# Kernel optimization log

Hardware: AMD Instinct MI355X
Metric: run time of the kernel (lower is better)

## Reference

```python
import jax, jax.numpy as jnp
import numpy as np

PART = 6
FEAT = 1024
DIM_CUT = 8
DC = FEAT // DIM_CUT  # 128
BATCH = 8192
NEG = -1000000.0
LRELU_SLOPE = 0.25
BN_EPS = 1e-5
L2_EPS = 1e-8


def lrelu(x):
    return jnp.where(x >= 0, x, LRELU_SLOPE * x)


def l2norm(x, axis=1):
    n = jnp.sqrt(jnp.sum(x * x, axis=axis, keepdims=True))
    return x / (n + L2_EPS)


def setup_inputs() -> dict:
    key = jax.random.key(0)
    ks = jax.random.split(key, 5)
    x = jax.random.normal(ks[0], (BATCH, FEAT, PART), dtype=jnp.float32)
    w_ps = jax.random.normal(ks[1], (PART, DC, FEAT), dtype=jnp.float32) * 0.02
    w_cs = jax.random.normal(ks[2], (PART, DC, FEAT), dtype=jnp.float32) * 0.02
    w_up = jax.random.normal(ks[3], (PART, FEAT, DC), dtype=jnp.float32) * 0.02
    w_la = jax.random.normal(ks[4], (PART, 512, FEAT), dtype=jnp.float32) * 0.02
    bn_gamma = jnp.ones((PART, FEAT), dtype=jnp.float32)
    bn_beta = jnp.zeros((PART, FEAT), dtype=jnp.float32)
    bn_mean = jnp.zeros((PART, FEAT), dtype=jnp.float32)
    bn_var = jnp.ones((PART, FEAT), dtype=jnp.float32)
    return {"x": x, "w_ps": w_ps, "w_cs": w_cs, "w_up": w_up,
            "bn_gamma": bn_gamma, "bn_beta": bn_beta,
            "bn_mean": bn_mean, "bn_var": bn_var, "w_la": w_la}


def reference(x, w_ps, w_cs, w_up, bn_gamma, bn_beta, bn_mean, bn_var, w_la):
    # x: [B, C=1024, P]. Per-part 1x1 convs == per-part matmuls, batched via einsum.
    ps = lrelu(jnp.einsum('bcp,pkc->bkp', x, w_ps))   # [B, 128, P]
    cs = lrelu(jnp.einsum('bcp,pkc->bkp', x, w_cs))   # [B, 128, P]
    ps_n = l2norm(ps, axis=1)
    cs_n = l2norm(cs, axis=1)
    # masked self-attention over parts
    att = jnp.einsum('bkp,bkq->bpq', ps_n, cs_n)       # [B, P, P]
    att = att + (jnp.eye(PART, dtype=att.dtype) * NEG)[None]
    att = jax.nn.softmax(att, axis=1)                  # torch F.softmax(dim=1)
    emb_att = jnp.einsum('bkp,bpq->bkq', ps_n, att)    # [B, 128, P]
    # per-part up-dim conv + BN(eval) + LReLU
    h = jnp.einsum('bkp,pok->bop', emb_att, w_up)      # [B, 1024, P]
    inv = 1.0 / jnp.sqrt(bn_var + BN_EPS)              # [P, 1024]
    h = (h - bn_mean.T[None]) * (bn_gamma * inv).T[None] + bn_beta.T[None]
    h = lrelu(h)
    emb2 = x + h                                       # residual, [B, 1024, P]
    # per-part local-attention conv (no BN / relu)
    out = jnp.einsum('bcp,poc->bop', emb2, w_la)       # [B, 512, P]
    return out
```

## Files before the change

kernel.cpp:

```cpp
#include <hip/hip_runtime.h>
#include <cstdint>
#include <cstddef>

#define B_N  8192
#define FEAT 1024
#define PART 6
#define DC   128
#define OUTC 512

typedef __bf16 bf16;
typedef bf16 bf16x8 __attribute__((ext_vector_type(8)));
typedef bf16 bf16x2 __attribute__((ext_vector_type(2)));
typedef float f32x4 __attribute__((ext_vector_type(4)));

__device__ __forceinline__ void gload16(const bf16* g, bf16* l) {
  __builtin_amdgcn_global_load_lds(
      (const __attribute__((address_space(1))) void*)g,
      (__attribute__((address_space(3))) void*)l, 16, 0, 0);
}

__global__ void k_prep(const float* __restrict__ w_ps, const float* __restrict__ w_cs,
                       const float* __restrict__ w_up, const float* __restrict__ w_la,
                       const float* __restrict__ g, const float* __restrict__ be,
                       const float* __restrict__ m, const float* __restrict__ v,
                       bf16* __restrict__ wpsb, bf16* __restrict__ wupb,
                       bf16* __restrict__ wlab, float* __restrict__ bnsc,
                       float* __restrict__ bnsh) {
  int i = blockIdx.x * 256 + threadIdx.x;
  const int NW = PART * DC * FEAT;
  const int NL = PART * OUTC * FEAT;
  if (i < NW) {
    int z = i / (DC * FEAT), r = i % (DC * FEAT);
    wpsb[(size_t)(2 * z) * DC * FEAT + r] = (bf16)w_ps[i];
    wpsb[(size_t)(2 * z + 1) * DC * FEAT + r] = (bf16)w_cs[i];
    wupb[i] = (bf16)w_up[i];
  }
  if (i < NL) wlab[i] = (bf16)w_la[i];
  if (i < PART * FEAT) {
    float inv = 1.0f / sqrtf(v[i] + 1e-5f);
    float s = g[i] * inv;
    bnsc[i] = s;
    bnsh[i] = be[i] - m[i] * s;
  }
}

__global__ void k_transpose_x(const float* __restrict__ x, bf16* __restrict__ xT) {
  int t = blockIdx.x * 256 + threadIdx.x;
  int b = t >> 9;
  int c0 = (t & 511) << 1;
  const float4* src = (const float4*)(x + ((size_t)b * FEAT + c0) * PART);
  float4 v0 = src[0], v1 = src[1], v2 = src[2];
  float e[12] = {v0.x, v0.y, v0.z, v0.w, v1.x, v1.y, v1.z, v1.w, v2.x, v2.y, v2.z, v2.w};
#pragma unroll
  for (int p = 0; p < PART; ++p) {
    bf16x2 w; w.x = (bf16)e[p]; w.y = (bf16)e[6 + p];
    *(bf16x2*)(xT + ((size_t)p * B_N + b) * FEAT + c0) = w;
  }
}

template <int EPI, int K, int N, int TM, int TN, int NZ>
__global__ __launch_bounds__(256) void k_gemm(
    const bf16* __restrict__ Abase, const bf16* __restrict__ Wbase,
    bf16* __restrict__ Out,
    const float* __restrict__ bnsc, const float* __restrict__ bnsh,
    const bf16* __restrict__ resid) {
  __shared__ bf16 As[128 * 64];
  __shared__ bf16 Ws[128 * 64];
  const int tid = threadIdx.x;
  const int wv = tid >> 6, lane = tid & 63;
  const int wr = wv >> 1, wc = wv & 1;
  const int l = lane & 15, hh = lane >> 4;

  constexpr int NWG = TM * TN * NZ;
  constexpr int QC = NWG / 8;
  int bid = blockIdx.x;
  int lid = (bid & 7) * QC + (bid >> 3);
  int tn = lid % TN;
  int tm = (lid / TN) % TM;
  int z = lid / (TN * TM);

  const bf16* A = Abase + (size_t)z * B_N * K + (size_t)tm * 128 * K;
  const bf16* W = Wbase + (size_t)z * N * K + (size_t)tn * 128 * K;

  f32x4 acc[4][4] = {};

  for (int kt = 0; kt < K / 64; ++kt) {
    __syncthreads();
#pragma unroll
    for (int it = 0; it < 4; ++it) {
      int s = it * 256 + wv * 64 + lane;
      int r = s >> 3;
      int c = (s & 7) ^ (r & 7);
      gload16(A + (size_t)r * K + kt * 64 + c * 8, &As[(it * 256 + wv * 64) * 8]);
      gload16(W + (size_t)r * K + kt * 64 + c * 8, &Ws[(it * 256 + wv * 64) * 8]);
    }
    asm volatile("s_waitcnt vmcnt(0)" ::: "memory");
    __syncthreads();
#pragma unroll
    for (int kk = 0; kk < 2; ++kk) {
      bf16x8 af[4], wf[4];
#pragma unroll
      for (int mi = 0; mi < 4; ++mi) {
        int row = wr * 64 + mi * 16 + l;
        int c = (kk * 4 + hh) ^ (row & 7);
        af[mi] = *(const bf16x8*)&As[row * 64 + c * 8];
      }
#pragma unroll
      for (int ni = 0; ni < 4; ++ni) {
        int row = wc * 64 + ni * 16 + l;
        int c = (kk * 4 + hh) ^ (row & 7);
        wf[ni] = *(const bf16x8*)&Ws[row * 64 + c * 8];
      }
#pragma unroll
      for (int mi = 0; mi < 4; ++mi)
#pragma unroll
        for (int ni = 0; ni < 4; ++ni)
          acc[mi][ni] = __builtin_amdgcn_mfma_f32_16x16x32_bf16(af[mi], wf[ni], acc[mi][ni], 0, 0, 0);
    }
  }

#pragma unroll
  for (int mi = 0; mi < 4; ++mi)
#pragma unroll
    for (int ni = 0; ni < 4; ++ni)
#pragma unroll
      for (int r = 0; r < 4; ++r) {
        int row = tm * 128 + wr * 64 + mi * 16 + hh * 4 + r;
        int col = tn * 128 + wc * 64 + ni * 16 + l;
        float v = acc[mi][ni][r];
        if constexpr (EPI == 0) {
          v = v >= 0.f ? v : 0.25f * v;
        } else if constexpr (EPI == 1) {
          v = v * bnsc[z * N + col] + bnsh[z * N + col];
          v = v >= 0.f ? v : 0.25f * v;
          v += (float)resid[((size_t)z * B_N + row) * N + col];
        }
        Out[((size_t)z * B_N + row) * N + col] = (bf16)v;
      }
}

__global__ __launch_bounds__(256) void k_att(const bf16* __restrict__ psb,
                                             bf16* __restrict__ embT) {
  int wv = threadIdx.x >> 6, lane = threadIdx.x & 63;
  int b = blockIdx.x * 4 + wv;
  float p0[6], p1[6], c0[6], c1[6];
#pragma unroll
  for (int p = 0; p < 6; ++p) {
    const bf16* base = psb + ((size_t)p * B_N + b) * 256;
    bf16x2 v = *(const bf16x2*)(base + 2 * lane);
    p0[p] = (float)v.x; p1[p] = (float)v.y;
    bf16x2 u = *(const bf16x2*)(base + 128 + 2 * lane);
    c0[p] = (float)u.x; c1[p] = (float)u.y;
  }
  float red[48];
#pragma unroll
  for (int p = 0; p < 6; ++p) {
    red[p] = p0[p] * p0[p] + p1[p] * p1[p];
    red[6 + p] = c0[p] * c0[p] + c1[p] * c1[p];
  }
#pragma unroll
  for (int p = 0; p < 6; ++p)
#pragma unroll
    for (int q = 0; q < 6; ++q)
      red[12 + p * 6 + q] = p0[p] * c0[q] + p1[p] * c1[q];
#pragma unroll
  for (int m = 1; m < 64; m <<= 1)
#pragma unroll
    for (int i = 0; i < 48; ++i)
      red[i] += __shfl_xor(red[i], m, 64);

  float inp[6], inc[6];
#pragma unroll
  for (int p = 0; p < 6; ++p) {
    inp[p] = 1.f / (sqrtf(red[p]) + 1e-8f);
    inc[p] = 1.f / (sqrtf(red[6 + p]) + 1e-8f);
  }
  float att[6][6];
#pragma unroll
  for (int p = 0; p < 6; ++p)
#pragma unroll
    for (int q = 0; q < 6; ++q)
      att[p][q] = red[12 + p * 6 + q] * inp[p] * inc[q] + (p == q ? -1000000.f : 0.f);
#pragma unroll
  for (int q = 0; q < 6; ++q) {
    float mx = att[0][q];
#pragma unroll
    for (int p = 1; p < 6; ++p) mx = fmaxf(mx, att[p][q]);
    float e[6], s = 0.f;
#pragma unroll
    for (int p = 0; p < 6; ++p) { e[p] = expf(att[p][q] - mx); s += e[p]; }
    float is = 1.f / s;
#pragma unroll
    for (int p = 0; p < 6; ++p) att[p][q] = e[p] * is;
  }
#pragma unroll
  for (int q = 0; q < 6; ++q) {
    float e0 = 0.f, e1 = 0.f;
#pragma unroll
    for (int p = 0; p < 6; ++p) {
      float a = att[p][q] * inp[p];
      e0 += p0[p] * a; e1 += p1[p] * a;
    }
    bf16x2 w; w.x = (bf16)e0; w.y = (bf16)e1;
    *(bf16x2*)(embT + ((size_t)q * B_N + b) * DC + 2 * lane) = w;
  }
}

__global__ void k_transpose_out(const bf16* __restrict__ oT, float* __restrict__ out) {
  int t = blockIdx.x * 256 + threadIdx.x;
  int b = t >> 8;
  int o0 = (t & 255) << 1;
  float a[6], c[6];
#pragma unroll
  for (int p = 0; p < 6; ++p) {
    bf16x2 v = *(const bf16x2*)(oT + ((size_t)p * B_N + b) * OUTC + o0);
    a[p] = (float)v.x; c[p] = (float)v.y;
  }
  float* dst = out + ((size_t)b * OUTC + o0) * PART;
  float4 w0 = {a[0], a[1], a[2], a[3]};
  float4 w1 = {a[4], a[5], c[0], c[1]};
  float4 w2 = {c[2], c[3], c[4], c[5]};
  ((float4*)dst)[0] = w0; ((float4*)dst)[1] = w1; ((float4*)dst)[2] = w2;
}

extern "C" void kernel_launch(void* const* d_in, const int* in_sizes, int n_in,
                              void* d_out, int out_size, void* d_ws, size_t ws_size,
                              hipStream_t stream) {
  const float* x    = (const float*)d_in[0];
  const float* w_ps = (const float*)d_in[1];
  const float* w_cs = (const float*)d_in[2];
  const float* w_up = (const float*)d_in[3];
  const float* gam  = (const float*)d_in[4];
  const float* bet  = (const float*)d_in[5];
  const float* mea  = (const float*)d_in[6];
  const float* var  = (const float*)d_in[7];
  const float* w_la = (const float*)d_in[8];

  char* ws = (char*)d_ws;
  size_t off = 0;
  auto alloc = [&](size_t bytes) { void* p = ws + off; off += (bytes + 255) & ~(size_t)255; return p; };

  bf16* xT    = (bf16*)alloc((size_t)PART * B_N * FEAT * 2);
  bf16* wpsb  = (bf16*)alloc((size_t)PART * 256 * FEAT * 2);
  bf16* wupb  = (bf16*)alloc((size_t)PART * FEAT * DC * 2);
  bf16* wlab  = (bf16*)alloc((size_t)PART * OUTC * FEAT * 2);
  float* bnsc = (float*)alloc((size_t)PART * FEAT * 4);
  float* bnsh = (float*)alloc((size_t)PART * FEAT * 4);
  bf16* psb   = (bf16*)alloc((size_t)PART * B_N * 256 * 2);
  bf16* embT  = (bf16*)alloc((size_t)PART * B_N * DC * 2);
  bf16* emb2T = (bf16*)alloc((size_t)PART * B_N * FEAT * 2);
  bf16* outT  = xT;

  k_prep<<<(PART * OUTC * FEAT + 255) / 256, 256, 0, stream>>>(
      w_ps, w_cs, w_up, w_la, gam, bet, mea, var, wpsb, wupb, wlab, bnsc, bnsh);
  k_transpose_x<<<B_N * 512 / 256, 256, 0, stream>>>(x, xT);

  k_gemm<0, FEAT, 256, 64, 2, 6><<<768, 256, 0, stream>>>(
      xT, wpsb, psb, nullptr, nullptr, nullptr);
  k_att<<<B_N / 4, 256, 0, stream>>>(psb, embT);
  k_gemm<1, DC, FEAT, 64, 8, 6><<<3072, 256, 0, stream>>>(
      embT, wupb, emb2T, bnsc, bnsh, xT);
  k_gemm<2, FEAT, OUTC, 64, 4, 6><<<1536, 256, 0, stream>>>(
      emb2T, wlab, outT, nullptr, nullptr, nullptr);
  k_transpose_out<<<B_N * 256 / 256, 256, 0, stream>>>(outT, (float*)d_out);
}
```

Before: 615.9 us.

## Double-buffer GEMM K-loop, fuse prep kernels, pack two batches per wave in attention

The GEMM main loop now uses two 32-wide K buffers in LDS. It prefetches the next tile with partial vmcnt waits and raw s_barrier, and drops the XOR swizzle for a layout split by half-wave. It also sets launch_bounds occupancy to 3. The weight-prep and x-transpose kernels are merged into one launch. The attention kernel packs two batch rows per wave with 4-element vector loads, halving the shuffle reduction depth, and uses fast __expf. The risks are LDS bank conflicts from the unswizzled layout and more barriers per K step.

Result: no change. 624.8 us (+1.5%).

```diff
diff --git a/kernel.cpp b/kernel.cpp
--- a/kernel.cpp
+++ b/kernel.cpp
@@ -10,6 +10,7 @@
 
 typedef __bf16 bf16;
 typedef bf16 bf16x8 __attribute__((ext_vector_type(8)));
+typedef bf16 bf16x4 __attribute__((ext_vector_type(4)));
 typedef bf16 bf16x2 __attribute__((ext_vector_type(2)));
 typedef float f32x4 __attribute__((ext_vector_type(4)));
 
@@ -19,53 +20,53 @@
       (__attribute__((address_space(3))) void*)l, 16, 0, 0);
 }
 
-__global__ void k_prep(const float* __restrict__ w_ps, const float* __restrict__ w_cs,
-                       const float* __restrict__ w_up, const float* __restrict__ w_la,
-                       const float* __restrict__ g, const float* __restrict__ be,
-                       const float* __restrict__ m, const float* __restrict__ v,
-                       bf16* __restrict__ wpsb, bf16* __restrict__ wupb,
-                       bf16* __restrict__ wlab, float* __restrict__ bnsc,
-                       float* __restrict__ bnsh) {
-  int i = blockIdx.x * 256 + threadIdx.x;
+__global__ void k_preptx(const float* __restrict__ x, bf16* __restrict__ xT,
+                         const float* __restrict__ w_ps, const float* __restrict__ w_cs,
+                         const float* __restrict__ w_up, const float* __restrict__ w_la,
+                         const float* __restrict__ g, const float* __restrict__ be,
+                         const float* __restrict__ m, const float* __restrict__ v,
+                         bf16* __restrict__ wpsb, bf16* __restrict__ wupb,
+                         bf16* __restrict__ wlab, float* __restrict__ bnsc,
+                         float* __restrict__ bnsh) {
+  int t = blockIdx.x * 256 + threadIdx.x;
+  {
+    int b = t >> 9;
+    int c0 = (t & 511) << 1;
+    const float4* src = (const float4*)(x + ((size_t)b * FEAT + c0) * PART);
+    float4 v0 = src[0], v1 = src[1], v2 = src[2];
+    float e[12] = {v0.x, v0.y, v0.z, v0.w, v1.x, v1.y, v1.z, v1.w, v2.x, v2.y, v2.z, v2.w};
+#pragma unroll
+    for (int p = 0; p < PART; ++p) {
+      bf16x2 w; w.x = (bf16)e[p]; w.y = (bf16)e[6 + p];
+      *(bf16x2*)(xT + ((size_t)p * B_N + b) * FEAT + c0) = w;
+    }
+  }
   const int NW = PART * DC * FEAT;
   const int NL = PART * OUTC * FEAT;
-  if (i < NW) {
-    int z = i / (DC * FEAT), r = i % (DC * FEAT);
-    wpsb[(size_t)(2 * z) * DC * FEAT + r] = (bf16)w_ps[i];
-    wpsb[(size_t)(2 * z + 1) * DC * FEAT + r] = (bf16)w_cs[i];
-    wupb[i] = (bf16)w_up[i];
-  }
-  if (i < NL) wlab[i] = (bf16)w_la[i];
-  if (i < PART * FEAT) {
-    float inv = 1.0f / sqrtf(v[i] + 1e-5f);
-    float s = g[i] * inv;
-    bnsc[i] = s;
-    bnsh[i] = be[i] - m[i] * s;
-  }
-}
-
-__global__ void k_transpose_x(const float* __restrict__ x, bf16* __restrict__ xT) {
-  int t = blockIdx.x * 256 + threadIdx.x;
-  int b = t >> 9;
-  int c0 = (t & 511) << 1;
-  const float4* src = (const float4*)(x + ((size_t)b * FEAT + c0) * PART);
-  float4 v0 = src[0], v1 = src[1], v2 = src[2];
-  float e[12] = {v0.x, v0.y, v0.z, v0.w, v1.x, v1.y, v1.z, v1.w, v2.x, v2.y, v2.z, v2.w};
-#pragma unroll
-  for (int p = 0; p < PART; ++p) {
-    bf16x2 w; w.x = (bf16)e[p]; w.y = (bf16)e[6 + p];
-    *(bf16x2*)(xT + ((size_t)p * B_N + b) * FEAT + c0) = w;
+  if (t < NW) {
+    int z = t / (DC * FEAT), r = t % (DC * FEAT);
+    wpsb[(size_t)(2 * z) * DC * FEAT + r] = (bf16)w_ps[t];
+    wpsb[(size_t)(2 * z + 1) * DC * FEAT + r] = (bf16)w_cs[t];
+    wupb[t] = (bf16)w_up[t];
+  }
+  if (t < NL) wlab[t] = (bf16)w_la[t];
+  if (t < PART * FEAT) {
+    float inv = 1.0f / sqrtf(v[t] + 1e-5f);
+    float s = g[t] * inv;
+    bnsc[t] = s;
+    bnsh[t] = be[t] - m[t] * s;
   }
 }
 
 template <int EPI, int K, int N, int TM, int TN, int NZ>
-__global__ __launch_bounds__(256) void k_gemm(
+__global__ __launch_bounds__(256, 3) void k_gemm(
     const bf16* __restrict__ Abase, const bf16* __restrict__ Wbase,
     bf16* __restrict__ Out,
     const float* __restrict__ bnsc, const float* __restrict__ bnsh,
     const bf16* __restrict__ resid) {
-  __shared__ bf16 As[128 * 64];
-  __shared__ bf16 Ws[128 * 64];
+  constexpr int NT = K / 32;
+  __shared__ bf16 As[2][4096];
+  __shared__ bf16 Ws[2][4096];
   const int tid = threadIdx.x;
   const int wv = tid >> 6, lane = tid & 63;
   const int wr = wv >> 1, wc = wv & 1;
@@ -84,39 +85,48 @@
 
   f32x4 acc[4][4] = {};
 
-  for (int kt = 0; kt < K / 64; ++kt) {
-    __syncthreads();
-#pragma unroll
-    for (int it = 0; it < 4; ++it) {
-      int s = it * 256 + wv * 64 + lane;
-      int r = s >> 3;
-      int c = (s & 7) ^ (r & 7);
-      gload16(A + (size_t)r * K + kt * 64 + c * 8, &As[(it * 256 + wv * 64) * 8]);
-      gload16(W + (size_t)r * K + kt * 64 + c * 8, &Ws[(it * 256 + wv * 64) * 8]);
-    }
-    asm volatile("s_waitcnt vmcnt(0)" ::: "memory");
-    __syncthreads();
-#pragma unroll
-    for (int kk = 0; kk < 2; ++kk) {
-      bf16x8 af[4], wf[4];
-#pragma unroll
-      for (int mi = 0; mi < 4; ++mi) {
-        int row = wr * 64 + mi * 16 + l;
-        int c = (kk * 4 + hh) ^ (row & 7);
-        af[mi] = *(const bf16x8*)&As[row * 64 + c * 8];
-      }
-#pragma unroll
-      for (int ni = 0; ni < 4; ++ni) {
-        int row = wc * 64 + ni * 16 + l;
-        int c = (kk * 4 + hh) ^ (row & 7);
-        wf[ni] = *(const bf16x8*)&Ws[row * 64 + c * 8];
-      }
-#pragma unroll
-      for (int mi = 0; mi < 4; ++mi)
-#pragma unroll
-        for (int ni = 0; ni < 4; ++ni)
-          acc[mi][ni] = __builtin_amdgcn_mfma_f32_16x16x32_bf16(af[mi], wf[ni], acc[mi][ni], 0, 0, 0);
-    }
+  auto STAGE = [&](int buf, int kt) {
+#pragma unroll
+    for (int it = 0; it < 2; ++it) {
+      int gidx = it * 4 + wv;
+      int row = (gidx & 1) * 64 + lane;
+      int chunk = gidx >> 1;
+      int slot0 = it * 256 + wv * 64;
+      gload16(A + (size_t)row * K + kt * 32 + chunk * 8, &As[buf][slot0 * 8]);
+      gload16(W + (size_t)row * K + kt * 32 + chunk * 8, &Ws[buf][slot0 * 8]);
+    }
+  };
+
+  STAGE(0, 0);
+  for (int kt = 0; kt < NT; ++kt) {
+    int cur = kt & 1;
+    if (kt + 1 < NT) {
+      STAGE(cur ^ 1, kt + 1);
+      asm volatile("s_waitcnt vmcnt(4)" ::: "memory");
+    } else {
+      asm volatile("s_waitcnt vmcnt(0)" ::: "memory");
+    }
+    __builtin_amdgcn_sched_barrier(0);
+    __builtin_amdgcn_s_barrier();
+    __builtin_amdgcn_sched_barrier(0);
+
+    bf16x8 af[4], wf[4];
+#pragma unroll
+    for (int mi = 0; mi < 4; ++mi)
+      af[mi] = *(const bf16x8*)&As[cur][(hh * 128 + wr * 64 + mi * 16 + l) * 8];
+#pragma unroll
+    for (int ni = 0; ni < 4; ++ni)
+      wf[ni] = *(const bf16x8*)&Ws[cur][(hh * 128 + wc * 64 + ni * 16 + l) * 8];
+#pragma unroll
+    for (int mi = 0; mi < 4; ++mi)
+#pragma unroll
+      for (int ni = 0; ni < 4; ++ni)
+        acc[mi][ni] = __builtin_amdgcn_mfma_f32_16x16x32_bf16(af[mi], wf[ni], acc[mi][ni], 0, 0, 0);
+
+    __builtin_amdgcn_sched_barrier(0);
+    asm volatile("" ::: "memory");
+    __builtin_amdgcn_s_barrier();
+    __builtin_amdgcn_sched_barrier(0);
   }
 
 #pragma unroll
@@ -142,67 +152,77 @@
 __global__ __launch_bounds__(256) void k_att(const bf16* __restrict__ psb,
                                              bf16* __restrict__ embT) {
   int wv = threadIdx.x >> 6, lane = threadIdx.x & 63;
-  int b = blockIdx.x * 4 + wv;
-  float p0[6], p1[6], c0[6], c1[6];
-#pragma unroll
-  for (int p = 0; p < 6; ++p) {
-    const bf16* base = psb + ((size_t)p * B_N + b) * 256;
-    bf16x2 v = *(const bf16x2*)(base + 2 * lane);
-    p0[p] = (float)v.x; p1[p] = (float)v.y;
-    bf16x2 u = *(const bf16x2*)(base + 128 + 2 * lane);
-    c0[p] = (float)u.x; c1[p] = (float)u.y;
+  int half = lane >> 5, sl = lane & 31;
+  int b = blockIdx.x * 8 + wv * 2 + half;
+  float p[6][4], c[6][4];
+#pragma unroll
+  for (int pp = 0; pp < 6; ++pp) {
+    const bf16* base = psb + ((size_t)pp * B_N + b) * 256;
+    bf16x4 vp = *(const bf16x4*)(base + 4 * sl);
+    bf16x4 vc = *(const bf16x4*)(base + 128 + 4 * sl);
+#pragma unroll
+    for (int j = 0; j < 4; ++j) { p[pp][j] = (float)vp[j]; c[pp][j] = (float)vc[j]; }
   }
   float red[48];
 #pragma unroll
-  for (int p = 0; p < 6; ++p) {
-    red[p] = p0[p] * p0[p] + p1[p] * p1[p];
-    red[6 + p] = c0[p] * c0[p] + c1[p] * c1[p];
-  }
-#pragma unroll
-  for (int p = 0; p < 6; ++p)
-#pragma unroll
-    for (int q = 0; q < 6; ++q)
-      red[12 + p * 6 + q] = p0[p] * c0[q] + p1[p] * c1[q];
-#pragma unroll
-  for (int m = 1; m < 64; m <<= 1)
+  for (int pp = 0; pp < 6; ++pp) {
+    float np = 0.f, nc = 0.f;
+#pragma unroll
+    for (int j = 0; j < 4; ++j) { np = fmaf(p[pp][j], p[pp][j], np); nc = fmaf(c[pp][j], c[pp][j], nc); }
+    red[pp] = np; red[6 + pp] = nc;
+  }
+#pragma unroll
+  for (int pp = 0; pp < 6; ++pp)
+#pragma unroll
+    for (int q = 0; q < 6; ++q) {
+      float d = 0.f;
+#pragma unroll
+      for (int j = 0; j < 4; ++j) d = fmaf(p[pp][j], c[q][j], d);
+      red[12 + pp * 6 + q] = d;
+    }
+#pragma unroll
+  for (int m = 1; m < 32; m <<= 1)
 #pragma unroll
     for (int i = 0; i < 48; ++i)
       red[i] += __shfl_xor(red[i], m, 64);
 
   float inp[6], inc[6];
 #pragma unroll
-  for (int p = 0; p < 6; ++p) {
-    inp[p] = 1.f / (sqrtf(red[p]) + 1e-8f);
-    inc[p] = 1.f / (sqrtf(red[6 + p]) + 1e-8f);
+  for (int pp = 0; pp < 6; ++pp) {
+    inp[pp] = 1.f / (sqrtf(red[pp]) + 1e-8f);
+    inc[pp] = 1.f / (sqrtf(red[6 + pp]) + 1e-8f);
   }
   float att[6][6];
 #pragma unroll
-  for (int p = 0; p < 6; ++p)
+  for (int pp = 0; pp < 6; ++pp)
 #pragma unroll
     for (int q = 0; q < 6; ++q)
-      att[p][q] = red[12 + p * 6 + q] * inp[p] * inc[q] + (p == q ? -1000000.f : 0.f);
+      att[pp][q] = red[12 + pp * 6 + q] * inp[pp] * inc[q] + (pp == q ? -1000000.f : 0.f);
 #pragma unroll
   for (int q = 0; q < 6; ++q) {
     float mx = att[0][q];
 #pragma unroll
-    for (int p = 1; p < 6; ++p) mx = fmaxf(mx, att[p][q]);
+    for (int pp = 1; pp < 6; ++pp) mx = fmaxf(mx, att[pp][q]);
     float e[6], s = 0.f;
 #pragma unroll
-    for (int p = 0; p < 6; ++p) { e[p] = expf(att[p][q] - mx); s += e[p]; }
+    for (int pp = 0; pp < 6; ++pp) { e[pp] = __expf(att[pp][q] - mx); s += e[pp]; }
     float is = 1.f / s;
 #pragma unroll
-    for (int p = 0; p < 6; ++p) att[p][q] = e[p] * is;
+    for (int pp = 0; pp < 6; ++pp) att[pp][q] = e[pp] * is;
   }
 #pragma unroll
   for (int q = 0; q < 6; ++q) {
-    float e0 = 0.f, e1 = 0.f;
-#pragma unroll
-    for (int p = 0; p < 6; ++p) {
-      float a = att[p][q] * inp[p];
-      e0 += p0[p] * a; e1 += p1[p] * a;
-    }
-    bf16x2 w; w.x = (bf16)e0; w.y = (bf16)e1;
-    *(bf16x2*)(embT + ((size_t)q * B_N + b) * DC + 2 * lane) = w;
+    float e[4] = {0.f, 0.f, 0.f, 0.f};
+#pragma unroll
+    for (int pp = 0; pp < 6; ++pp) {
+      float a = att[pp][q] * inp[pp];
+#pragma unroll
+      for (int j = 0; j < 4; ++j) e[j] = fmaf(p[pp][j], a, e[j]);
+    }
+    bf16x4 w;
+#pragma unroll
+    for (int j = 0; j < 4; ++j) w[j] = (bf16)e[j];
+    *(bf16x4*)(embT + ((size_t)q * B_N + b) * DC + 4 * sl) = w;
   }
 }
 
@@ -251,13 +271,12 @@
   bf16* emb2T = (bf16*)alloc((size_t)PART * B_N * FEAT * 2);
   bf16* outT  = xT;
 
-  k_prep<<<(PART * OUTC * FEAT + 255) / 256, 256, 0, stream>>>(
-      w_ps, w_cs, w_up, w_la, gam, bet, mea, var, wpsb, wupb, wlab, bnsc, bnsh);
-  k_transpose_x<<<B_N * 512 / 256, 256, 0, stream>>>(x, xT);
+  k_preptx<<<B_N * 512 / 256, 256, 0, stream>>>(
+      x, xT, w_ps, w_cs, w_up, w_la, gam, bet, mea, var, wpsb, wupb, wlab, bnsc, bnsh);
 
   k_gemm<0, FEAT, 256, 64, 2, 6><<<768, 256, 0, stream>>>(
       xT, wpsb, psb, nullptr, nullptr, nullptr);
-  k_att<<<B_N / 4, 256, 0, stream>>>(psb, embT);
+  k_att<<<B_N / 8, 256, 0, stream>>>(psb, embT);
   k_gemm<1, DC, FEAT, 64, 8, 6><<<3072, 256, 0, stream>>>(
       embT, wupb, emb2T, bnsc, bnsh, xT);
   k_gemm<2, FEAT, OUTC, 64, 4, 6><<<1536, 256, 0, stream>>>(
```
